# Kernel optimization log

Measured on AMD Instinct MI355X. Metric: run time of the kernel, lower is better.

## Reference

```python
import jax, jax.numpy as jnp
import numpy as np

NUM_NODES_G1 = 60000
NUM_NODES_G2 = 50000
NUM_REL = 16
NUM_BASES = 4
DIM = 128  # node_dim == hidden_dim == final_dim
L_COMMON = 100


def _concept_layer(x, edge_index):
    # Gather-based concept propagation: x_i <- x_i + mean_{j in N(i)} x_j
    src, dst = edge_index[0], edge_index[1]
    n = x.shape[0]
    agg = jax.ops.segment_sum(x[src], dst, num_segments=n)
    deg = jax.ops.segment_sum(jnp.ones((src.shape[0],), x.dtype), dst, num_segments=n)
    return x + agg / jnp.clip(deg, 1.0)[:, None]


def _rgcn_layer(x, edge_index, edge_type, basis, comp, root, bias):
    # Basis-decomposed RGCN: out_i = x_i @ root + bias + sum_r (1/|N_i^r|) sum_{j in N_i^r} x_j @ W_r,
    # W_r = sum_b comp[r,b] * basis[b]. Reorder: scatter comp-weighted x[src] per basis, then one GEMM per basis.
    src, dst = edge_index[0], edge_index[1]
    n = x.shape[0]
    e = src.shape[0]
    seg = dst * NUM_REL + edge_type  # per-(node, relation) bucket
    cnt = jax.ops.segment_sum(jnp.ones((e,), x.dtype), seg, num_segments=n * NUM_REL)
    norm = 1.0 / jnp.clip(cnt, 1.0)
    coef = comp[edge_type] * norm[seg][:, None]  # [E, B]
    xsrc = x[src]  # [E, D] -- dominant gather traffic
    out = x @ root + bias
    for b in range(NUM_BASES):  # small fixed loop over bases
        agg_b = jax.ops.segment_sum(xsrc * coef[:, b:b + 1], dst, num_segments=n)
        out = out + agg_b @ basis[b]
    return out


def setup_inputs() -> dict:
    key = jax.random.key(0)
    ks = jax.random.split(key, 16)
    e2, e1 = 800000, 800000
    return {
        "edge_index_g2": jax.random.randint(ks[0], (2, e2), 0, NUM_NODES_G2),
        "edge_type_g2": jax.random.randint(ks[1], (e2,), 0, NUM_REL),
        "edge_index_g1": jax.random.randint(ks[2], (2, e1), 0, NUM_NODES_G1),
        "left_common": jax.random.randint(ks[3], (L_COMMON,), 0, NUM_NODES_G1),
        "all_node_embedding": jax.random.normal(ks[4], (NUM_NODES_G1, DIM), jnp.float32),
        "basis1": jax.random.normal(ks[5], (NUM_BASES, DIM, DIM), jnp.float32) * 0.05,
        "comp1": jax.random.normal(ks[6], (NUM_REL, NUM_BASES), jnp.float32),
        "root1": jax.random.normal(ks[7], (DIM, DIM), jnp.float32) * 0.05,
        "bias1": jnp.zeros((DIM,), jnp.float32),
        "basis2": jax.random.normal(ks[8], (NUM_BASES, DIM, DIM), jnp.float32) * 0.05,
        "comp2": jax.random.normal(ks[9], (NUM_REL, NUM_BASES), jnp.float32),
        "root2": jax.random.normal(ks[10], (DIM, DIM), jnp.float32) * 0.05,
        "bias2": jnp.zeros((DIM,), jnp.float32),
        "weights": jax.random.uniform(ks[11], (DIM, 1), jnp.float32),
    }


def reference(edge_index_g2, edge_type_g2, edge_index_g1, left_common,
              all_node_embedding, basis1, comp1, root1, bias1,
              basis2, comp2, root2, bias2, weights):
    x_g1 = jax.nn.relu(_concept_layer(all_node_embedding, edge_index_g1))
    x = x_g1[:NUM_NODES_G2]
    x = _rgcn_layer(x, edge_index_g2, edge_type_g2, basis1, comp1, root1, bias1)
    x = jax.nn.relu(x)  # relu_use == 1
    x_g2 = _rgcn_layer(x, edge_index_g2, edge_type_g2, basis2, comp2, root2, bias2)
    ty = x_g1[left_common]  # [L, D]
    # mul_def outer elementwise product followed by matmul with weights collapses to one contraction:
    # logits[n,l] = sum_d x_g2[n,d] * ty[l,d] * w[d]
    logits = jnp.einsum('nd,ld,d->nl', x_g2, ty, weights[:, 0])
    return jax.nn.softmax(logits, axis=1)
```

## Files before the change

kernel.cpp:

```cpp
#include <hip/hip_runtime.h>
#include <hip/hip_bf16.h>
#include <math.h>

#define N1 60000
#define N2 50000
#define DIM 128
#define NREL 16
#define NB 4
#define LCOM 100
#define LPAD 112

typedef __attribute__((ext_vector_type(8))) short short8;
typedef __attribute__((ext_vector_type(4))) float f32x4;
typedef __attribute__((ext_vector_type(4))) _Float16 half4;

__device__ __forceinline__ float bf2f(unsigned short u) {
    union { unsigned int i; float f; } c; c.i = ((unsigned int)u) << 16; return c.f;
}
__device__ __forceinline__ unsigned short f2bf(float f) {
    union { float f; unsigned int i; } c; c.f = f;
    unsigned int r = c.i + 0x7FFF + ((c.i >> 16) & 1);
    return (unsigned short)(r >> 16);
}
__device__ __forceinline__ void split8(float4 a, float4 b, short8& h, short8& l) {
    float f[8] = {a.x, a.y, a.z, a.w, b.x, b.y, b.z, b.w};
#pragma unroll
    for (int j = 0; j < 8; j++) {
        unsigned short hh = f2bf(f[j]);
        h[j] = (short)hh;
        l[j] = (short)f2bf(f[j] - bf2f(hh));
    }
}

__global__ __launch_bounds__(256) void k_prelude(
        const int* __restrict__ ei1, int E1, int* __restrict__ deg1, int HB1,
        const int* __restrict__ ei2, int E2, int* __restrict__ deg2, int HB2,
        const float* __restrict__ root1, const float* __restrict__ basis1,
        unsigned short* __restrict__ Wh1, unsigned short* __restrict__ Wl1,
        const float* __restrict__ root2, const float* __restrict__ basis2,
        unsigned short* __restrict__ Wh2, unsigned short* __restrict__ Wl2, int PB,
        const float* __restrict__ emb, _Float16* __restrict__ embh, int n4) {
    int b = blockIdx.x;
    if (b < HB1) {
        int e0 = b * 1024 + threadIdx.x;
#pragma unroll
        for (int j = 0; j < 4; j++) {
            int e = e0 + j * 256;
            if (e < E1) atomicAdd(deg1 + ei1[E1 + e], 1);
        }
    } else if (b < HB1 + HB2) {
        int e0 = (b - HB1) * 1024 + threadIdx.x;
#pragma unroll
        for (int j = 0; j < 4; j++) {
            int e = e0 + j * 256;
            if (e < E2) atomicAdd(deg2 + ei2[E2 + e], 1);
        }
    } else if (b < HB1 + HB2 + PB) {
        int t = (b - HB1 - HB2) * 256 + threadIdx.x;
        if (t < 2 * 640 * 128) {
            int which = t >= 640 * 128;
            int tt = which ? t - 640 * 128 : t;
            const float* root = which ? root2 : root1;
            const float* basis = which ? basis2 : basis1;
            unsigned short* Wh = which ? Wh2 : Wh1;
            unsigned short* Wl = which ? Wl2 : Wl1;
            int k = tt >> 7, n = tt & 127;
            float v = (k < 128) ? root[k * 128 + n] : basis[(k - 128) * 128 + n];
            unsigned short h = f2bf(v);
            Wh[n * 640 + k] = h;
            Wl[n * 640 + k] = f2bf(v - bf2f(h));
        }
    } else {
        int i = (b - HB1 - HB2 - PB) * 256 + threadIdx.x;
        if (i < n4) {
            float4 v = ((const float4*)emb)[i];
            half4 o = {(_Float16)v.x, (_Float16)v.y, (_Float16)v.z, (_Float16)v.w};
            ((half4*)embh)[i] = o;
        }
    }
}

__global__ __launch_bounds__(256) void k_scan_p1m(const int* __restrict__ inA, int nA, int nbA,
                                                  int* __restrict__ bsumA,
                                                  const int* __restrict__ inB, int nB,
                                                  int* __restrict__ bsumB) {
    __shared__ int red[256];
    const int* in; int n; int* bsum; int b;
    if ((int)blockIdx.x < nbA) { in = inA; n = nA; bsum = bsumA; b = blockIdx.x; }
    else { in = inB; n = nB; bsum = bsumB; b = blockIdx.x - nbA; }
    int base = b * 1024;
    int tid = threadIdx.x;
    int s = 0;
#pragma unroll
    for (int j = 0; j < 4; j++) {
        int i = base + tid * 4 + j;
        if (i < n) s += in[i];
    }
    red[tid] = s;
    __syncthreads();
    for (int d = 128; d; d >>= 1) {
        if (tid < d) red[tid] += red[tid + d];
        __syncthreads();
    }
    if (tid == 0) bsum[b] = red[0];
}

__global__ __launch_bounds__(64) void k_scan_p2m(const int* __restrict__ bsumA, int* __restrict__ boffA,
                                                 int* __restrict__ offA, int nbA, int nA,
                                                 const int* __restrict__ bsumB, int* __restrict__ boffB,
                                                 int* __restrict__ offB, int nbB, int nB) {
    __shared__ int s[64];
    const int* bsum; int* boff; int* off; int nb; int n;
    if (blockIdx.x == 0) { bsum = bsumA; boff = boffA; off = offA; nb = nbA; n = nA; }
    else { bsum = bsumB; boff = boffB; off = offB; nb = nbB; n = nB; }
    int tid = threadIdx.x;
    int v = (tid < nb) ? bsum[tid] : 0;
    s[tid] = v;
    __syncthreads();
    for (int d = 1; d < 64; d <<= 1) {
        int t = (tid >= d) ? s[tid - d] : 0;
        __syncthreads();
        s[tid] += t;
        __syncthreads();
    }
    if (tid < nb) boff[tid] = s[tid] - v;
    if (tid == 63) off[n] = s[63];
}

__global__ __launch_bounds__(256) void k_scan_p3m(const int* __restrict__ inA, const int* __restrict__ boffA,
                                                  int* __restrict__ offA, int* __restrict__ curA,
                                                  int nA, int nbA,
                                                  const int* __restrict__ inB, const int* __restrict__ boffB,
                                                  int* __restrict__ offB, int* __restrict__ curB, int nB) {
    __shared__ int red[256];
    const int* in; const int* boff; int* off; int* cur; int n; int b;
    if ((int)blockIdx.x < nbA) { in = inA; boff = boffA; off = offA; cur = curA; n = nA; b = blockIdx.x; }
    else { in = inB; boff = boffB; off = offB; cur = curB; n = nB; b = blockIdx.x - nbA; }
    int base = b * 1024;
    int tid = threadIdx.x;
    int v[4];
    int s = 0;
#pragma unroll
    for (int j = 0; j < 4; j++) {
        int i = base + tid * 4 + j;
        v[j] = (i < n) ? in[i] : 0;
        s += v[j];
    }
    red[tid] = s;
    __syncthreads();
    for (int d = 1; d < 256; d <<= 1) {
        int t = (tid >= d) ? red[tid - d] : 0;
        __syncthreads();
        red[tid] += t;
        __syncthreads();
    }
    int run = boff[b] + red[tid] - s;
#pragma unroll
    for (int j = 0; j < 4; j++) {
        int i = base + tid * 4 + j;
        if (i < n) {
            off[i] = run; cur[i] = run;
            run += v[j];
        }
    }
}

__global__ void k_scat1(const int* __restrict__ ei, int E, int* __restrict__ cur,
                        int* __restrict__ elist) {
    int e0 = blockIdx.x * 1024 + threadIdx.x;
#pragma unroll
    for (int j = 0; j < 4; j++) {
        int e = e0 + j * 256;
        if (e < E) {
            int pos = atomicAdd(cur + ei[E + e], 1);
            elist[pos] = ei[e];
        }
    }
}

__global__ __launch_bounds__(256) void k_mix(
        const _Float16* __restrict__ embh, const float* __restrict__ emb,
        const int* __restrict__ off1, const int* __restrict__ elist1,
        float* __restrict__ xg1, _Float16* __restrict__ xg1h, int CONC_B,
        const int* __restrict__ ei2, const int* __restrict__ et2, int E2,
        int* __restrict__ cur2, int* __restrict__ elist2, int SC2_B,
        const int* __restrict__ lc, const float* __restrict__ w,
        unsigned short* __restrict__ tyh, unsigned short* __restrict__ tyl) {
    int b = blockIdx.x;
    if (b < CONC_B) {
        int node = b * 4 + (threadIdx.x >> 6);
        int lane = threadIdx.x & 63;
        if (node >= N2) return;
        int half = lane >> 5, d4 = (lane & 31) * 4;
        int s0 = off1[node], s1 = off1[node + 1];
        float4 acc = {0.f, 0.f, 0.f, 0.f};
        int i = s0;
        for (; i + 4 <= s1; i += 4) {
            int sa = elist1[i + half];
            int sb = elist1[i + 2 + half];
            half4 ha = *(const half4*)(embh + (size_t)sa * DIM + d4);
            half4 hb = *(const half4*)(embh + (size_t)sb * DIM + d4);
            acc.x += (float)ha[0] + (float)hb[0];
            acc.y += (float)ha[1] + (float)hb[1];
            acc.z += (float)ha[2] + (float)hb[2];
            acc.w += (float)ha[3] + (float)hb[3];
        }
        for (; i < s1; i += 2) {
            int e = i + half;
            bool ok = e < s1;
            int s = elist1[ok ? e : i];
            half4 hv = *(const half4*)(embh + (size_t)s * DIM + d4);
            if (ok) {
                acc.x += (float)hv[0]; acc.y += (float)hv[1];
                acc.z += (float)hv[2]; acc.w += (float)hv[3];
            }
        }
        acc.x += __shfl_xor(acc.x, 32, 64);
        acc.y += __shfl_xor(acc.y, 32, 64);
        acc.z += __shfl_xor(acc.z, 32, 64);
        acc.w += __shfl_xor(acc.w, 32, 64);
        if (half == 0) {
            float inv = 1.0f / (float)max(s1 - s0, 1);
            float4 e = *(const float4*)(emb + (size_t)node * DIM + d4);
            float4 o = {fmaxf(e.x + acc.x * inv, 0.f), fmaxf(e.y + acc.y * inv, 0.f),
                        fmaxf(e.z + acc.z * inv, 0.f), fmaxf(e.w + acc.w * inv, 0.f)};
            *(float4*)(xg1 + (size_t)node * DIM + d4) = o;
            half4 oh = {(_Float16)o.x, (_Float16)o.y, (_Float16)o.z, (_Float16)o.w};
            *(half4*)(xg1h + (size_t)node * DIM + d4) = oh;
        }
    } else if (b < CONC_B + SC2_B) {
        int e0 = (b - CONC_B) * 1024 + threadIdx.x;
#pragma unroll
        for (int j = 0; j < 4; j++) {
            int e = e0 + j * 256;
            if (e < E2) {
                int pos = atomicAdd(cur2 + ei2[E2 + e], 1);
                elist2[pos] = (ei2[e] << 4) | et2[e];
            }
        }
    } else {
        if (threadIdx.x >= 64) return;
        int l = b - CONC_B - SC2_B;
        int lane = threadIdx.x;
        int d0 = lane * 2;
        if (l >= LCOM) {
            ushort2 z = {0, 0};
            *(ushort2*)(tyh + (size_t)l * 128 + d0) = z;
            *(ushort2*)(tyl + (size_t)l * 128 + d0) = z;
            return;
        }
        int row = lc[l];
        int s0 = off1[row], s1 = off1[row + 1];
        float2 acc = {0.f, 0.f};
        for (int i = s0; i < s1; i++) {
            int s = elist1[i];
            float2 v = *(const float2*)(emb + (size_t)s * DIM + lane * 2);
            acc.x += v.x; acc.y += v.y;
        }
        float inv = 1.0f / (float)max(s1 - s0, 1);
        float2 e = *(const float2*)(emb + (size_t)row * DIM + lane * 2);
        float v0 = fmaxf(e.x + acc.x * inv, 0.f) * w[d0];
        float v1 = fmaxf(e.y + acc.y * inv, 0.f) * w[d0 + 1];
        unsigned short h0 = f2bf(v0), h1 = f2bf(v1);
        ushort2 hh = {h0, h1};
        ushort2 ll = {f2bf(v0 - bf2f(h0)), f2bf(v1 - bf2f(h1))};
        *(ushort2*)(tyh + (size_t)l * 128 + d0) = hh;
        *(ushort2*)(tyl + (size_t)l * 128 + d0) = ll;
    }
}

__global__ __launch_bounds__(256) void k_rgcn_gather(const _Float16* __restrict__ xh,
                                                     const int* __restrict__ off,
                                                     const int* __restrict__ elist,
                                                     const float* __restrict__ comp,
                                                     float* __restrict__ agg, int n) {
    __shared__ float scomp[NREL * NB];
    __shared__ float nrmlds[4][NREL];
    if (threadIdx.x < NREL * NB) scomp[threadIdx.x] = comp[threadIdx.x];
    __syncthreads();
    int nb = threadIdx.x >> 6;
    int node = blockIdx.x * 4 + nb;
    int lane = threadIdx.x & 63;
    if (node >= n) return;
    int s0 = off[node], s1 = off[node + 1];
    unsigned long long c0 = 0, c1 = 0;
    for (int i = s0 + lane; i < s1; i += 64) {
        int t = elist[i] & 15;
        if (t < 8) c0 += 1ull << (8 * t); else c1 += 1ull << (8 * (t - 8));
    }
#pragma unroll
    for (int o = 32; o; o >>= 1) {
        c0 += __shfl_xor(c0, o, 64);
        c1 += __shfl_xor(c1, o, 64);
    }
    if (lane < NREL) {
        unsigned int c = (lane < 8) ? (unsigned int)((c0 >> (8 * lane)) & 255)
                                    : (unsigned int)((c1 >> (8 * (lane - 8))) & 255);
        nrmlds[nb][lane] = 1.0f / (float)max(c, 1u);
    }
    int half = lane >> 5, d4 = (lane & 31) * 4;
    float4 a0 = {0, 0, 0, 0}, a1 = a0, a2 = a0, a3 = a0;
    int i = s0;
#define RG_EDGE(E_IDX, GATE)                                                   \
    {                                                                          \
        int p = elist[E_IDX];                                                  \
        int s = p >> 4, t = p & 15;                                            \
        float nr = nrmlds[nb][t] * (GATE);                                     \
        float4 cf = *(const float4*)(scomp + t * 4);                           \
        half4 hv = *(const half4*)(xh + (size_t)s * DIM + d4);                 \
        float4 v = {(float)hv[0], (float)hv[1], (float)hv[2], (float)hv[3]};   \
        float c0_ = cf.x * nr, c1_ = cf.y * nr, c2_ = cf.z * nr, c3_ = cf.w * nr; \
        a0.x = fmaf(c0_, v.x, a0.x); a0.y = fmaf(c0_, v.y, a0.y);              \
        a0.z = fmaf(c0_, v.z, a0.z); a0.w = fmaf(c0_, v.w, a0.w);              \
        a1.x = fmaf(c1_, v.x, a1.x); a1.y = fmaf(c1_, v.y, a1.y);              \
        a1.z = fmaf(c1_, v.z, a1.z); a1.w = fmaf(c1_, v.w, a1.w);              \
        a2.x = fmaf(c2_, v.x, a2.x); a2.y = fmaf(c2_, v.y, a2.y);              \
        a2.z = fmaf(c2_, v.z, a2.z); a2.w = fmaf(c2_, v.w, a2.w);              \
        a3.x = fmaf(c3_, v.x, a3.x); a3.y = fmaf(c3_, v.y, a3.y);              \
        a3.z = fmaf(c3_, v.z, a3.z); a3.w = fmaf(c3_, v.w, a3.w);              \
    }
    for (; i + 4 <= s1; i += 4) {
        RG_EDGE(i + half, 1.0f);
        RG_EDGE(i + 2 + half, 1.0f);
    }
    for (; i < s1; i += 2) {
        int e = i + half;
        bool ok = e < s1;
        int ei_ = ok ? e : i;
        RG_EDGE(ei_, ok ? 1.0f : 0.0f);
    }
#undef RG_EDGE
    a0.x += __shfl_xor(a0.x, 32, 64); a0.y += __shfl_xor(a0.y, 32, 64);
    a0.z += __shfl_xor(a0.z, 32, 64); a0.w += __shfl_xor(a0.w, 32, 64);
    a1.x += __shfl_xor(a1.x, 32, 64); a1.y += __shfl_xor(a1.y, 32, 64);
    a1.z += __shfl_xor(a1.z, 32, 64); a1.w += __shfl_xor(a1.w, 32, 64);
    a2.x += __shfl_xor(a2.x, 32, 64); a2.y += __shfl_xor(a2.y, 32, 64);
    a2.z += __shfl_xor(a2.z, 32, 64); a2.w += __shfl_xor(a2.w, 32, 64);
    a3.x += __shfl_xor(a3.x, 32, 64); a3.y += __shfl_xor(a3.y, 32, 64);
    a3.z += __shfl_xor(a3.z, 32, 64); a3.w += __shfl_xor(a3.w, 32, 64);
    if (half == 0) {
        float* o = agg + (size_t)node * (NB * DIM) + d4;
        *(float4*)(o + 0 * DIM) = a0;
        *(float4*)(o + 1 * DIM) = a1;
        *(float4*)(o + 2 * DIM) = a2;
        *(float4*)(o + 3 * DIM) = a3;
    }
}

#define LDSK 40
__global__ __launch_bounds__(256) void k_gemm(const float* __restrict__ x,
                                              const float* __restrict__ agg,
                                              const unsigned short* __restrict__ Wh,
                                              const unsigned short* __restrict__ Wl,
                                              const float* __restrict__ bias,
                                              float* __restrict__ out,
                                              _Float16* __restrict__ out_h, int relu) {
    __shared__ __align__(16) short Ah[128 * LDSK];
    __shared__ __align__(16) short Al[128 * LDSK];
    __shared__ __align__(16) short Bh[128 * LDSK];
    __shared__ __align__(16) short Bl[128 * LDSK];
    int tid = threadIdx.x;
    int lane = tid & 63, wid = tid >> 6;
    int wave_m = wid >> 1, wave_n = wid & 1;
    int l15 = lane & 15, quad = lane >> 4;
    int row0 = blockIdx.x * 128;

    int srow = tid >> 1, skh = (tid & 1) * 16;

    f32x4 acc[4][4] = {};
    for (int k0 = 0; k0 < 640; k0 += 32) {
        {
            int rg = row0 + srow;
            float4 q0 = {0, 0, 0, 0}, q1 = q0, q2 = q0, q3 = q0;
            if (rg < N2) {
                const float* src = (k0 < 128) ? (x + (size_t)rg * 128 + k0 + skh)
                                              : (agg + (size_t)rg * 512 + (k0 - 128) + skh);
                q0 = *(const float4*)(src + 0);
                q1 = *(const float4*)(src + 4);
                q2 = *(const float4*)(src + 8);
                q3 = *(const float4*)(src + 12);
            }
            short8 h0, l0, h1, l1;
            split8(q0, q1, h0, l0);
            split8(q2, q3, h1, l1);
            *(short8*)(&Ah[srow * LDSK + skh]) = h0;
            *(short8*)(&Ah[srow * LDSK + skh + 8]) = h1;
            *(short8*)(&Al[srow * LDSK + skh]) = l0;
            *(short8*)(&Al[srow * LDSK + skh + 8]) = l1;
        }
        {
            const unsigned short* sh = Wh + (size_t)srow * 640 + k0 + skh;
            const unsigned short* sl = Wl + (size_t)srow * 640 + k0 + skh;
            *(short8*)(&Bh[srow * LDSK + skh]) = *(const short8*)(sh);
            *(short8*)(&Bh[srow * LDSK + skh + 8]) = *(const short8*)(sh + 8);
            *(short8*)(&Bl[srow * LDSK + skh]) = *(const short8*)(sl);
            *(short8*)(&Bl[srow * LDSK + skh + 8]) = *(const short8*)(sl + 8);
        }
        __syncthreads();
        short8 ah[4], al[4], bh[4], bl[4];
#pragma unroll
        for (int i = 0; i < 4; i++) {
            int ro = (wave_m * 64 + i * 16 + l15) * LDSK + quad * 8;
            ah[i] = *(const short8*)(&Ah[ro]);
            al[i] = *(const short8*)(&Al[ro]);
        }
#pragma unroll
        for (int j = 0; j < 4; j++) {
            int ro = (wave_n * 64 + j * 16 + l15) * LDSK + quad * 8;
            bh[j] = *(const short8*)(&Bh[ro]);
            bl[j] = *(const short8*)(&Bl[ro]);
        }
#pragma unroll
        for (int i = 0; i < 4; i++)
#pragma unroll
            for (int j = 0; j < 4; j++) {
                acc[i][j] = __builtin_amdgcn_mfma_f32_16x16x32_bf16(al[i], bh[j], acc[i][j], 0, 0, 0);
                acc[i][j] = __builtin_amdgcn_mfma_f32_16x16x32_bf16(ah[i], bl[j], acc[i][j], 0, 0, 0);
                acc[i][j] = __builtin_amdgcn_mfma_f32_16x16x32_bf16(ah[i], bh[j], acc[i][j], 0, 0, 0);
            }
        __syncthreads();
    }
#pragma unroll
    for (int j = 0; j < 4; j++) {
        int gcol = wave_n * 64 + j * 16 + l15;
        float bv = bias[gcol];
#pragma unroll
        for (int i = 0; i < 4; i++) {
            int grow_base = row0 + wave_m * 64 + i * 16 + quad * 4;
#pragma unroll
            for (int r = 0; r < 4; r++) {
                int grow = grow_base + r;
                if (grow >= N2) continue;
                float v = acc[i][j][r] + bv;
                if (relu) v = fmaxf(v, 0.f);
                out[(size_t)grow * 128 + gcol] = v;
                if (out_h) out_h[(size_t)grow * 128 + gcol] = (_Float16)v;
            }
        }
    }
}

__global__ __launch_bounds__(256) void k_logits(const float* __restrict__ h2,
                                                const unsigned short* __restrict__ tyh,
                                                const unsigned short* __restrict__ tyl,
                                                float* __restrict__ out, int M) {
    int wid = threadIdx.x >> 6, lane = threadIdx.x & 63;
    int l15 = lane & 15, quad = lane >> 4;
    int row0w = blockIdx.x * 64 + wid * 16;
    int arow = min(row0w + l15, M - 1);
    f32x4 acc[7] = {};
#pragma unroll
    for (int k0 = 0; k0 < 128; k0 += 32) {
        const float* ap = h2 + (size_t)arow * 128 + k0 + quad * 8;
        float4 q0 = *(const float4*)(ap);
        float4 q1 = *(const float4*)(ap + 4);
        short8 ah, al;
        split8(q0, q1, ah, al);
#pragma unroll
        for (int j = 0; j < 7; j++) {
            size_t bo = (size_t)(j * 16 + l15) * 128 + k0 + quad * 8;
            short8 bh = *(const short8*)(tyh + bo);
            short8 bl = *(const short8*)(tyl + bo);
            acc[j] = __builtin_amdgcn_mfma_f32_16x16x32_bf16(al, bh, acc[j], 0, 0, 0);
            acc[j] = __builtin_amdgcn_mfma_f32_16x16x32_bf16(ah, bl, acc[j], 0, 0, 0);
            acc[j] = __builtin_amdgcn_mfma_f32_16x16x32_bf16(ah, bh, acc[j], 0, 0, 0);
        }
    }
    bool v6 = (l15 < LCOM - 96);
#pragma unroll
    for (int r = 0; r < 4; r++) {
        int grow = row0w + quad * 4 + r;
        float m = -INFINITY;
#pragma unroll
        for (int j = 0; j < 6; j++) m = fmaxf(m, acc[j][r]);
        if (v6) m = fmaxf(m, acc[6][r]);
        m = fmaxf(m, __shfl_xor(m, 8, 64));
        m = fmaxf(m, __shfl_xor(m, 4, 64));
        m = fmaxf(m, __shfl_xor(m, 2, 64));
        m = fmaxf(m, __shfl_xor(m, 1, 64));
        float e[7];
        float s = 0.f;
#pragma unroll
        for (int j = 0; j < 6; j++) { e[j] = __expf(acc[j][r] - m); s += e[j]; }
        e[6] = v6 ? __expf(acc[6][r] - m) : 0.f;
        s += e[6];
        s += __shfl_xor(s, 8, 64);
        s += __shfl_xor(s, 4, 64);
        s += __shfl_xor(s, 2, 64);
        s += __shfl_xor(s, 1, 64);
        float inv = 1.0f / s;
        if (grow < M) {
#pragma unroll
            for (int j = 0; j < 6; j++) out[(size_t)grow * LCOM + j * 16 + l15] = e[j] * inv;
            if (v6) out[(size_t)grow * LCOM + 96 + l15] = e[6] * inv;
        }
    }
}

extern "C" void kernel_launch(void* const* d_in, const int* in_sizes, int n_in,
                              void* d_out, int out_size, void* d_ws, size_t ws_size,
                              hipStream_t stream) {
    const int* ei2 = (const int*)d_in[0];
    const int* et2 = (const int*)d_in[1];
    const int* ei1 = (const int*)d_in[2];
    const int* lc = (const int*)d_in[3];
    const float* emb = (const float*)d_in[4];
    const float* basis1 = (const float*)d_in[5];
    const float* comp1 = (const float*)d_in[6];
    const float* root1 = (const float*)d_in[7];
    const float* bias1 = (const float*)d_in[8];
    const float* basis2 = (const float*)d_in[9];
    const float* comp2 = (const float*)d_in[10];
    const float* root2 = (const float*)d_in[11];
    const float* bias2 = (const float*)d_in[12];
    const float* wts = (const float*)d_in[13];
    float* out = (float*)d_out;
    int E2 = in_sizes[0] / 2, E1 = in_sizes[2] / 2;

    float* ws = (float*)d_ws;
    float* xg1 = ws;
    float* h1 = xg1 + 6400000;
    float* agg = h1 + 6400000;
    _Float16* emb_h = (_Float16*)(agg + 25600000);
    unsigned short* tyh = (unsigned short*)(emb_h + 7680000);
    unsigned short* tyl = tyh + LPAD * 128;
    unsigned short* Wh1 = tyl + LPAD * 128;
    unsigned short* Wl1 = Wh1 + 81920;
    unsigned short* Wh2 = Wl1 + 81920;
    unsigned short* Wl2 = Wh2 + 81920;
    int* ipool = (int*)(Wl2 + 81920);
    int* deg1 = ipool;
    int* deg2 = deg1 + 60000;
    int* off1 = deg2 + 50000;
    int* cur1 = off1 + 60001;
    int* elist1 = cur1 + 60000;
    int* off2 = elist1 + 800000;
    int* cur2 = off2 + 50001;
    int* elist2 = cur2 + 50000;
    int* bsum1 = elist2 + 800000;
    int* boff1 = bsum1 + 64;
    int* bsum2 = boff1 + 64;
    int* boff2 = bsum2 + 64;
    _Float16* xg1_h = (_Float16*)h1;
    _Float16* h1_h = emb_h;
    float* h2 = xg1;

    const int NB1 = (N1 + 1023) / 1024;
    const int NB2 = (N2 + 1023) / 1024;
    const int HB1 = (E1 + 1023) / 1024;
    const int HB2 = (E2 + 1023) / 1024;
    const int PB = (2 * 640 * 128) / 256;
    const int CB = (N1 * DIM / 4 + 255) / 256;
    const int CONC_B = (N2 + 3) / 4;
    const int SC2_B = HB2;

    hipMemsetAsync(deg1, 0, (60000 + 50000) * sizeof(int), stream);

    k_prelude<<<HB1 + HB2 + PB + CB, 256, 0, stream>>>(
        ei1, E1, deg1, HB1, ei2, E2, deg2, HB2,
        root1, basis1, Wh1, Wl1, root2, basis2, Wh2, Wl2, PB,
        emb, emb_h, N1 * DIM / 4);

    k_scan_p1m<<<NB1 + NB2, 256, 0, stream>>>(deg1, N1, NB1, bsum1, deg2, N2, bsum2);
    k_scan_p2m<<<2, 64, 0, stream>>>(bsum1, boff1, off1, NB1, N1, bsum2, boff2, off2, NB2, N2);
    k_scan_p3m<<<NB1 + NB2, 256, 0, stream>>>(deg1, boff1, off1, cur1, N1, NB1,
                                              deg2, boff2, off2, cur2, N2);

    k_scat1<<<HB1, 256, 0, stream>>>(ei1, E1, cur1, elist1);

    k_mix<<<CONC_B + SC2_B + LPAD, 256, 0, stream>>>(
        emb_h, emb, off1, elist1, xg1, xg1_h, CONC_B,
        ei2, et2, E2, cur2, elist2, SC2_B,
        lc, wts, tyh, tyl);

    k_rgcn_gather<<<CONC_B, 256, 0, stream>>>(xg1_h, off2, elist2, comp1, agg, N2);
    k_gemm<<<(N2 + 127) / 128, 256, 0, stream>>>(xg1, agg, Wh1, Wl1, bias1, h1, h1_h, 1);

    k_rgcn_gather<<<CONC_B, 256, 0, stream>>>(h1_h, off2, elist2, comp2, agg, N2);
    k_gemm<<<(N2 + 127) / 128, 256, 0, stream>>>(h1, agg, Wh2, Wl2, bias2, h2, (_Float16*)nullptr, 0);

    k_logits<<<(N2 + 63) / 64, 256, 0, stream>>>(h2, tyh, tyl, out, N2);
}
```

Measured before the change: 563.5 us.

## Merge both edge scatters into one kernel and halve GEMM row tile

The graph-2 edge bucketing moves out of the mixed concept-layer kernel and into one launch alongside the graph-1 scatter, so the concept kernel runs only gather work. The RGCN GEMM tile shrinks from 128 to 64 rows per block, which doubles the grid (about 782 blocks) for better occupancy and load balance across CUs. The cost is that each B-weight tile is reloaded by twice as many blocks, and the scatter kernels now compete for atomics in the same launch.

```diff
diff --git a/kernel.cpp b/kernel.cpp
--- a/kernel.cpp
+++ b/kernel.cpp
@@ -165,15 +165,30 @@
     }
 }
 
-__global__ void k_scat1(const int* __restrict__ ei, int E, int* __restrict__ cur,
-                        int* __restrict__ elist) {
-    int e0 = blockIdx.x * 1024 + threadIdx.x;
-#pragma unroll
-    for (int j = 0; j < 4; j++) {
-        int e = e0 + j * 256;
-        if (e < E) {
-            int pos = atomicAdd(cur + ei[E + e], 1);
-            elist[pos] = ei[e];
+__global__ void k_scat_both(const int* __restrict__ ei1, int E1, int* __restrict__ cur1,
+                            int* __restrict__ elist1, int SB1,
+                            const int* __restrict__ ei2, const int* __restrict__ et2, int E2,
+                            int* __restrict__ cur2, int* __restrict__ elist2) {
+    int b = blockIdx.x;
+    if (b < SB1) {
+        int e0 = b * 1024 + threadIdx.x;
+#pragma unroll
+        for (int j = 0; j < 4; j++) {
+            int e = e0 + j * 256;
+            if (e < E1) {
+                int pos = atomicAdd(cur1 + ei1[E1 + e], 1);
+                elist1[pos] = ei1[e];
+            }
+        }
+    } else {
+        int e0 = (b - SB1) * 1024 + threadIdx.x;
+#pragma unroll
+        for (int j = 0; j < 4; j++) {
+            int e = e0 + j * 256;
+            if (e < E2) {
+                int pos = atomicAdd(cur2 + ei2[E2 + e], 1);
+                elist2[pos] = (ei2[e] << 4) | et2[e];
+            }
         }
     }
 }
@@ -182,8 +197,6 @@
         const _Float16* __restrict__ embh, const float* __restrict__ emb,
         const int* __restrict__ off1, const int* __restrict__ elist1,
         float* __restrict__ xg1, _Float16* __restrict__ xg1h, int CONC_B,
-        const int* __restrict__ ei2, const int* __restrict__ et2, int E2,
-        int* __restrict__ cur2, int* __restrict__ elist2, int SC2_B,
         const int* __restrict__ lc, const float* __restrict__ w,
         unsigned short* __restrict__ tyh, unsigned short* __restrict__ tyl) {
     int b = blockIdx.x;
@@ -228,19 +241,9 @@
             half4 oh = {(_Float16)o.x, (_Float16)o.y, (_Float16)o.z, (_Float16)o.w};
             *(half4*)(xg1h + (size_t)node * DIM + d4) = oh;
         }
-    } else if (b < CONC_B + SC2_B) {
-        int e0 = (b - CONC_B) * 1024 + threadIdx.x;
-#pragma unroll
-        for (int j = 0; j < 4; j++) {
-            int e = e0 + j * 256;
-            if (e < E2) {
-                int pos = atomicAdd(cur2 + ei2[E2 + e], 1);
-                elist2[pos] = (ei2[e] << 4) | et2[e];
-            }
-        }
     } else {
         if (threadIdx.x >= 64) return;
-        int l = b - CONC_B - SC2_B;
+        int l = b - CONC_B;
         int lane = threadIdx.x;
         int d0 = lane * 2;
         if (l >= LCOM) {
@@ -355,52 +358,48 @@
                                               const float* __restrict__ bias,
                                               float* __restrict__ out,
                                               _Float16* __restrict__ out_h, int relu) {
-    __shared__ __align__(16) short Ah[128 * LDSK];
-    __shared__ __align__(16) short Al[128 * LDSK];
+    __shared__ __align__(16) short Ah[64 * LDSK];
+    __shared__ __align__(16) short Al[64 * LDSK];
     __shared__ __align__(16) short Bh[128 * LDSK];
     __shared__ __align__(16) short Bl[128 * LDSK];
     int tid = threadIdx.x;
     int lane = tid & 63, wid = tid >> 6;
-    int wave_m = wid >> 1, wave_n = wid & 1;
+    int wave_m = wid & 1, wave_n = wid >> 1;
     int l15 = lane & 15, quad = lane >> 4;
-    int row0 = blockIdx.x * 128;
-
-    int srow = tid >> 1, skh = (tid & 1) * 16;
-
-    f32x4 acc[4][4] = {};
+    int row0 = blockIdx.x * 64;
+
+    int arow_s = tid >> 2, akh = (tid & 3) * 8;
+    int brow_s = tid >> 1, bkh = (tid & 1) * 16;
+
+    f32x4 acc[2][4] = {};
     for (int k0 = 0; k0 < 640; k0 += 32) {
         {
-            int rg = row0 + srow;
-            float4 q0 = {0, 0, 0, 0}, q1 = q0, q2 = q0, q3 = q0;
+            int rg = row0 + arow_s;
+            float4 q0 = {0, 0, 0, 0}, q1 = q0;
             if (rg < N2) {
-                const float* src = (k0 < 128) ? (x + (size_t)rg * 128 + k0 + skh)
-                                              : (agg + (size_t)rg * 512 + (k0 - 128) + skh);
+                const float* src = (k0 < 128) ? (x + (size_t)rg * 128 + k0 + akh)
+                                              : (agg + (size_t)rg * 512 + (k0 - 128) + akh);
                 q0 = *(const float4*)(src + 0);
                 q1 = *(const float4*)(src + 4);
-                q2 = *(const float4*)(src + 8);
-                q3 = *(const float4*)(src + 12);
             }
-            short8 h0, l0, h1, l1;
+            short8 h0, l0;
             split8(q0, q1, h0, l0);
-            split8(q2, q3, h1, l1);
-            *(short8*)(&Ah[srow * LDSK + skh]) = h0;
-            *(short8*)(&Ah[srow * LDSK + skh + 8]) = h1;
-            *(short8*)(&Al[srow * LDSK + skh]) = l0;
-            *(short8*)(&Al[srow * LDSK + skh + 8]) = l1;
+            *(short8*)(&Ah[arow_s * LDSK + akh]) = h0;
+            *(short8*)(&Al[arow_s * LDSK + akh]) = l0;
         }
         {
-            const unsigned short* sh = Wh + (size_t)srow * 640 + k0 + skh;
-            const unsigned short* sl = Wl + (size_t)srow * 640 + k0 + skh;
-            *(short8*)(&Bh[srow * LDSK + skh]) = *(const short8*)(sh);
-            *(short8*)(&Bh[srow * LDSK + skh + 8]) = *(const short8*)(sh + 8);
-            *(short8*)(&Bl[srow * LDSK + skh]) = *(const short8*)(sl);
-            *(short8*)(&Bl[srow * LDSK + skh + 8]) = *(const short8*)(sl + 8);
-        }
-        __syncthreads();
-        short8 ah[4], al[4], bh[4], bl[4];
-#pragma unroll
-        for (int i = 0; i < 4; i++) {
-            int ro = (wave_m * 64 + i * 16 + l15) * LDSK + quad * 8;
+            const unsigned short* sh = Wh + (size_t)brow_s * 640 + k0 + bkh;
+            const unsigned short* sl = Wl + (size_t)brow_s * 640 + k0 + bkh;
+            *(short8*)(&Bh[brow_s * LDSK + bkh]) = *(const short8*)(sh);
+            *(short8*)(&Bh[brow_s * LDSK + bkh + 8]) = *(const short8*)(sh + 8);
+            *(short8*)(&Bl[brow_s * LDSK + bkh]) = *(const short8*)(sl);
+            *(short8*)(&Bl[brow_s * LDSK + bkh + 8]) = *(const short8*)(sl + 8);
+        }
+        __syncthreads();
+        short8 ah[2], al[2], bh[4], bl[4];
+#pragma unroll
+        for (int i = 0; i < 2; i++) {
+            int ro = (wave_m * 32 + i * 16 + l15) * LDSK + quad * 8;
             ah[i] = *(const short8*)(&Ah[ro]);
             al[i] = *(const short8*)(&Al[ro]);
         }
@@ -411,7 +410,7 @@
             bl[j] = *(const short8*)(&Bl[ro]);
         }
 #pragma unroll
-        for (int i = 0; i < 4; i++)
+        for (int i = 0; i < 2; i++)
 #pragma unroll
             for (int j = 0; j < 4; j++) {
                 acc[i][j] = __builtin_amdgcn_mfma_f32_16x16x32_bf16(al[i], bh[j], acc[i][j], 0, 0, 0);
@@ -425,8 +424,8 @@
         int gcol = wave_n * 64 + j * 16 + l15;
         float bv = bias[gcol];
 #pragma unroll
-        for (int i = 0; i < 4; i++) {
-            int grow_base = row0 + wave_m * 64 + i * 16 + quad * 4;
+        for (int i = 0; i < 2; i++) {
+            int grow_base = row0 + wave_m * 32 + i * 16 + quad * 4;
 #pragma unroll
             for (int r = 0; r < 4; r++) {
                 int grow = grow_base + r;
@@ -552,7 +551,6 @@
     const int PB = (2 * 640 * 128) / 256;
     const int CB = (N1 * DIM / 4 + 255) / 256;
     const int CONC_B = (N2 + 3) / 4;
-    const int SC2_B = HB2;
 
     hipMemsetAsync(deg1, 0, (60000 + 50000) * sizeof(int), stream);
 
@@ -566,18 +564,17 @@
     k_scan_p3m<<<NB1 + NB2, 256, 0, stream>>>(deg1, boff1, off1, cur1, N1, NB1,
                                               deg2, boff2, off2, cur2, N2);
 
-    k_scat1<<<HB1, 256, 0, stream>>>(ei1, E1, cur1, elist1);
-
-    k_mix<<<CONC_B + SC2_B + LPAD, 256, 0, stream>>>(
-        emb_h, emb, off1, elist1, xg1, xg1_h, CONC_B,
-        ei2, et2, E2, cur2, elist2, SC2_B,
-        lc, wts, tyh, tyl);
+    k_scat_both<<<HB1 + HB2, 256, 0, stream>>>(ei1, E1, cur1, elist1, HB1,
+                                               ei2, et2, E2, cur2, elist2);
+
+    k_mix<<<CONC_B + LPAD, 256, 0, stream>>>(
+        emb_h, emb, off1, elist1, xg1, xg1_h, CONC_B, lc, wts, tyh, tyl);
 
     k_rgcn_gather<<<CONC_B, 256, 0, stream>>>(xg1_h, off2, elist2, comp1, agg, N2);
-    k_gemm<<<(N2 + 127) / 128, 256, 0, stream>>>(xg1, agg, Wh1, Wl1, bias1, h1, h1_h, 1);
+    k_gemm<<<(N2 + 63) / 64, 256, 0, stream>>>(xg1, agg, Wh1, Wl1, bias1, h1, h1_h, 1);
 
     k_rgcn_gather<<<CONC_B, 256, 0, stream>>>(h1_h, off2, elist2, comp2, agg, N2);
-    k_gemm<<<(N2 + 127) / 128, 256, 0, stream>>>(h1, agg, Wh2, Wl2, bias2, h2, (_Float16*)nullptr, 0);
+    k_gemm<<<(N2 + 63) / 64, 256, 0, stream>>>(h1, agg, Wh2, Wl2, bias2, h2, (_Float16*)nullptr, 0);
 
     k_logits<<<(N2 + 63) / 64, 256, 0, stream>>>(h2, tyh, tyl, out, N2);
 }
```

Result: slower. 580.7 us (+3.1%).
